# Kernel tuning notes

Hardware: AMD Instinct MI355X
Metric: run time of the kernel (lower is better)

The kernel has to match this reference:

```python
import jax, jax.numpy as jnp
import numpy as np

D_MODEL = 1024
N_HEADS = 16
D_K = D_MODEL // N_HEADS


def setup_inputs() -> dict:
    key = jax.random.key(0)
    ks = jax.random.split(key, 9)
    B, S = 2, 2048
    scale = 1.0 / np.sqrt(D_MODEL)
    inp = {
        "X": jax.random.normal(ks[0], (B, S, D_MODEL), dtype=jnp.float32),
        "Wq": jax.random.normal(ks[1], (D_MODEL, D_MODEL), dtype=jnp.float32) * scale,
        "bq": jnp.zeros((D_MODEL,), dtype=jnp.float32),
        "Wk": jax.random.normal(ks[2], (D_MODEL, D_MODEL), dtype=jnp.float32) * scale,
        "bk": jnp.zeros((D_MODEL,), dtype=jnp.float32),
        "Wv": jax.random.normal(ks[3], (D_MODEL, D_MODEL), dtype=jnp.float32) * scale,
        "bv": jnp.zeros((D_MODEL,), dtype=jnp.float32),
        "Wo": jax.random.normal(ks[4], (D_MODEL, D_MODEL), dtype=jnp.float32) * scale,
        "bo": jnp.zeros((D_MODEL,), dtype=jnp.float32),
    }
    return inp


def reference(X, Wq, bq, Wk, bk, Wv, bv, Wo, bo):
    B, S, _ = X.shape
    # QKV projections (torch Linear: x @ W.T + b; here W stored as [in, out])
    Q = X @ Wq + bq
    K = X @ Wk + bk
    V = X @ Wv + bv
    # [B, S, H, Dk] -> [B, H, S, Dk]
    def split_heads(t):
        return t.reshape(B, S, N_HEADS, D_K).transpose(0, 2, 1, 3)
    Q, K, V = split_heads(Q), split_heads(K), split_heads(V)
    scores = jnp.einsum('bhqd,bhkd->bhqk', Q, K) / jnp.sqrt(jnp.float32(D_K))
    attn = jax.nn.softmax(scores, axis=-1)
    out = jnp.einsum('bhqk,bhkd->bhqd', attn, V)  # [B, H, S, Dk]
    out = out.transpose(0, 2, 1, 3).reshape(B, S, D_MODEL)
    return out @ Wo + bo
```

## Files before the change

### kernel.cpp

```cpp
#include <hip/hip_runtime.h>
#include <hip/hip_bf16.h>


typedef __attribute__((ext_vector_type(8))) short short8;
typedef __attribute__((ext_vector_type(4))) float f32x4;
typedef __attribute__((ext_vector_type(2))) float f32x2;
typedef unsigned short u16;
typedef unsigned int u32;

static __device__ __forceinline__ u16 f2bf(float f) {
    union { float f; u32 u; } c; c.f = f;
    u32 u = c.u;
    u32 r = u + 0x7fffu + ((u >> 16) & 1u);
    return (u16)(r >> 16);
}
static __device__ __forceinline__ float bf2f(u16 x) {
    union { u32 u; float f; } c; c.u = ((u32)x) << 16;
    return c.f;
}

#define GL1(p) ((const __attribute__((address_space(1))) void*)(p))
#define LD3(p) ((__attribute__((address_space(3))) void*)(p))
static __device__ __forceinline__ void gld16(const void* g, void* l) {
    __builtin_amdgcn_global_load_lds(GL1(g), LD3(l), 16, 0, 0);
}

#define Q_PRESCALE 0.18033688011112042f

__global__ __launch_bounds__(256) void prep(
    const float* __restrict__ X, u16* __restrict__ Xb,
    const float* __restrict__ Wq, const float* __restrict__ Wk,
    const float* __restrict__ Wv, const float* __restrict__ Wo,
    const float* __restrict__ bq, const float* __restrict__ bk,
    const float* __restrict__ bv,
    u16* __restrict__ Wqkv, u16* __restrict__ Wto, float* __restrict__ Bp)
{
    int id = blockIdx.x;
    int t = threadIdx.x;
    if (id == 5120) {
        for (int i = t; i < 3072; i += 256) {
            int wsel = i >> 10, c = i & 1023;
            float v = (wsel == 0) ? bq[c] * Q_PRESCALE : (wsel == 1 ? bk[c] : bv[c]);
            Bp[i] = v;
        }
        return;
    }
    if (id >= 1024) {
        int i = (id - 1024) * 1024 + t * 4;
        float4 v = *reinterpret_cast<const float4*>(X + i);
        ushort4 o;
        o.x = f2bf(v.x); o.y = f2bf(v.y); o.z = f2bf(v.z); o.w = f2bf(v.w);
        *reinterpret_cast<ushort4*>(Xb + i) = o;
        return;
    }
    int which = id >> 8;
    const float* W; u16* T; float sc;
    switch (which) {
        case 0: W = Wq; T = Wqkv;                sc = Q_PRESCALE; break;
        case 1: W = Wk; T = Wqkv + 1024 * 1024;  sc = 1.0f; break;
        case 2: W = Wv; T = Wqkv + 2048 * 1024;  sc = 1.0f; break;
        default: W = Wo; T = Wto;                sc = 1.0f; break;
    }
    int rem = id & 255;
    int n0 = (rem & 15) * 64, k0 = (rem >> 4) * 64;
    __shared__ float tile[64][65];
    int r = t / 16, c4 = (t % 16) * 4;
    #pragma unroll
    for (int p = 0; p < 4; p++) {
        int row = p * 16 + r;
        float4 v = *reinterpret_cast<const float4*>(W + (k0 + row) * 1024 + n0 + c4);
        tile[row][c4 + 0] = v.x * sc; tile[row][c4 + 1] = v.y * sc;
        tile[row][c4 + 2] = v.z * sc; tile[row][c4 + 3] = v.w * sc;
    }
    __syncthreads();
    #pragma unroll
    for (int p = 0; p < 4; p++) {
        int nrow = p * 16 + r;
        ushort4 o;
        o.x = f2bf(tile[c4 + 0][nrow]); o.y = f2bf(tile[c4 + 1][nrow]);
        o.z = f2bf(tile[c4 + 2][nrow]); o.w = f2bf(tile[c4 + 3][nrow]);
        *reinterpret_cast<ushort4*>(T + (n0 + nrow) * 1024 + k0 + c4) = o;
    }
}

__global__ __launch_bounds__(256, 3) void gemm_qkv(
    const u16* __restrict__ Xb, const u16* __restrict__ Wqkv,
    const float* __restrict__ Bp,
    u16* __restrict__ Qb, u16* __restrict__ Kb, u16* __restrict__ Vtg)
{
    __shared__ __align__(16) u16 As[2][128 * 32];
    __shared__ __align__(16) u16 Bs[2][128 * 32];
    int t = threadIdx.x;
    int w = t >> 6, lane = t & 63, l15 = lane & 15, quad = lane >> 4;
    int wm = (w >> 1) * 64, wn = (w & 1) * 64;
    int bid = blockIdx.x;
    int row0 = (bid & 31) * 128, col0 = (bid >> 5) * 128;

    int drow = lane >> 2;
    int gc8 = ((lane & 3) ^ (drow & 3) ^ ((drow >> 2) & 3)) * 8;
    int asw = ((quad ^ (l15 & 3) ^ ((l15 >> 2) & 3)) & 3) * 8;

    const u16* Ag = Xb + (row0 + drow) * 1024 + gc8;
    const u16* Bg = Wqkv + (col0 + drow) * 1024 + gc8;

    f32x4 acc[4][4];
    #pragma unroll
    for (int i = 0; i < 4; i++)
        #pragma unroll
        for (int j = 0; j < 4; j++)
            acc[i][j] = (f32x4){0.f, 0.f, 0.f, 0.f};

    #pragma unroll
    for (int q = 0; q < 2; q++) {
        int rr = w * 32 + q * 16;
        gld16(Ag + rr * 1024, &As[0][rr * 32]);
        gld16(Bg + rr * 1024, &Bs[0][rr * 32]);
    }
    for (int kt = 0; kt < 32; kt++) {
        __syncthreads();
        int cur = kt & 1;
        if (kt < 31) {
            int k0 = (kt + 1) * 32;
            #pragma unroll
            for (int q = 0; q < 2; q++) {
                int rr = w * 32 + q * 16;
                gld16(Ag + rr * 1024 + k0, &As[cur ^ 1][rr * 32]);
                gld16(Bg + rr * 1024 + k0, &Bs[cur ^ 1][rr * 32]);
            }
        }
        short8 a[4], b[4];
        #pragma unroll
        for (int i = 0; i < 4; i++)
            a[i] = *reinterpret_cast<const short8*>(&As[cur][(wm + i * 16 + l15) * 32 + asw]);
        #pragma unroll
        for (int j = 0; j < 4; j++)
            b[j] = *reinterpret_cast<const short8*>(&Bs[cur][(wn + j * 16 + l15) * 32 + asw]);
        #pragma unroll
        for (int i = 0; i < 4; i++)
            #pragma unroll
            for (int j = 0; j < 4; j++)
                acc[i][j] = __builtin_amdgcn_mfma_f32_16x16x32_bf16(a[i], b[j], acc[i][j], 0, 0, 0);
    }

    int osel = col0 >> 10;
    if (osel == 2) {
        #pragma unroll
        for (int i = 0; i < 4; i++) {
            int gr = row0 + wm + i * 16 + quad * 4;
            int b_ = gr >> 11, s = gr & 2047;
            #pragma unroll
            for (int j = 0; j < 4; j++) {
                int col = col0 + wn + j * 16 + l15;
                int c = col & 1023, h = c >> 6, d = c & 63;
                float bb = Bp[col];
                ushort4 pk;
                pk.x = f2bf(acc[i][j][0] + bb);
                pk.y = f2bf(acc[i][j][1] + bb);
                pk.z = f2bf(acc[i][j][2] + bb);
                pk.w = f2bf(acc[i][j][3] + bb);
                *reinterpret_cast<ushort4*>(&Vtg[((b_ * 16 + h) * 64 + d) * 2048 + s]) = pk;
            }
        }
    } else {
        u16* dst = osel ? Kb : Qb;
        #pragma unroll
        for (int i = 0; i < 4; i++) {
            int rowb = row0 + wm + i * 16 + quad * 4;
            #pragma unroll
            for (int j = 0; j < 4; j++) {
                int col = col0 + wn + j * 16 + l15;
                int c = col & 1023, h = c >> 6, d = c & 63;
                float bb = Bp[col];
                #pragma unroll
                for (int r = 0; r < 4; r++) {
                    int gr = rowb + r;
                    int b_ = gr >> 11, s = gr & 2047;
                    dst[(((b_ << 4) + h) * 2048 + s) * 64 + d] = f2bf(acc[i][j][r] + bb);
                }
            }
        }
    }
}

__global__ __launch_bounds__(256) void attn(
    const u16* __restrict__ Qb, const u16* __restrict__ Kb,
    const u16* __restrict__ Vtg, u16* __restrict__ Opart, float* __restrict__ Lsum)
{
    int bid = blockIdx.x;
    int bh = bid & 31, sp = (bid >> 5) & 3, qt = bid >> 7;
    int b_ = bh >> 4, h = bh & 15;
    const u16* Qp = Qb + bh * (2048 * 64);
    const u16* Kp = Kb + bh * (2048 * 64);
    const u16* Vp = Vtg + bh * (64 * 2048);
    u16* Op = Opart + sp * (4096 * 1024);
    float* Lp = Lsum + sp * (32 * 2048) + bh * 2048;

    __shared__ __align__(16) u16 Ks[64 * 64];
    __shared__ __align__(16) u16 Vt[64 * 64];
    __shared__ __align__(16) u16 Ps[128 * 64];

    int t = threadIdx.x, w = t >> 6, lane = t & 63, l15 = lane & 15, quad = lane >> 4;

    short8 qf[2][2];
    #pragma unroll
    for (int f = 0; f < 2; f++)
        #pragma unroll
        for (int ds = 0; ds < 2; ds++)
            qf[f][ds] = *reinterpret_cast<const short8*>(
                &Qp[(qt * 128 + w * 32 + f * 16 + l15) * 64 + ds * 32 + quad * 8]);

    int di = lane >> 3;
    int dc8 = ((lane & 7) ^ di) * 8;

    int rl = l15 & 7, rh = l15 >> 3;
    int koff[4][2];
    #pragma unroll
    for (int j = 0; j < 4; j++)
        #pragma unroll
        for (int ds = 0; ds < 2; ds++)
            koff[j][ds] = (j * 2 + rh) * 512 + rl * 64 + (((ds * 4 + quad) ^ rl) & 7) * 8;

    int pwt[2][4];
    #pragma unroll
    for (int f = 0; f < 2; f++)
        #pragma unroll
        for (int j = 0; j < 4; j++)
            pwt[f][j] = (w * 32 + f * 16 + l15) * 64 +
                        (((2 * j + (quad >> 1)) ^ rl) * 8) + (quad & 1) * 4;
    int prt[2][2];
    #pragma unroll
    for (int f = 0; f < 2; f++)
        #pragma unroll
        for (int ks = 0; ks < 2; ks++)
            prt[f][ks] = (w * 32 + f * 16 + l15) * 64 + (((4 * ks + quad) ^ rl) * 8);

    f32x4 acc[2][4];
    f32x2 lsum2[2] = {(f32x2){0.f, 0.f}, (f32x2){0.f, 0.f}};
    #pragma unroll
    for (int f = 0; f < 2; f++)
        #pragma unroll
        for (int j = 0; j < 4; j++) acc[f][j] = (f32x4){0.f, 0.f, 0.f, 0.f};

    int kb0 = sp * 512;

#define ISSUE_K(KB)                                                          \
    {                                                                        \
        _Pragma("unroll")                                                    \
        for (int sg = 0; sg < 2; sg++) {                                     \
            int seg = w * 2 + sg;                                            \
            gld16(&Kp[((KB) + seg * 8 + di) * 64 + dc8], &Ks[seg * 512]);    \
        }                                                                    \
    }
#define ISSUE_V(KB)                                                          \
    {                                                                        \
        _Pragma("unroll")                                                    \
        for (int sg = 0; sg < 2; sg++) {                                     \
            int seg = w * 2 + sg;                                            \
            gld16(&Vp[(seg * 8 + di) * 2048 + (KB) + dc8], &Vt[seg * 512]);  \
        }                                                                    \
    }

    ISSUE_K(kb0);
    ISSUE_V(kb0);
    __syncthreads();

    for (int kt = 0; kt < 8; kt++) {
        f32x4 sc[2][4];
        __builtin_amdgcn_s_setprio(1);
        #pragma unroll
        for (int j = 0; j < 4; j++) {
            f32x4 s0 = (f32x4){0.f, 0.f, 0.f, 0.f};
            f32x4 s1 = (f32x4){0.f, 0.f, 0.f, 0.f};
            #pragma unroll
            for (int ds = 0; ds < 2; ds++) {
                short8 kf = *reinterpret_cast<const short8*>(&Ks[koff[j][ds]]);
                s0 = __builtin_amdgcn_mfma_f32_16x16x32_bf16(kf, qf[0][ds], s0, 0, 0, 0);
                s1 = __builtin_amdgcn_mfma_f32_16x16x32_bf16(kf, qf[1][ds], s1, 0, 0, 0);
            }
            sc[0][j] = s0; sc[1][j] = s1;
        }
        __builtin_amdgcn_s_setprio(0);

        __syncthreads();
        if (kt < 7)
            ISSUE_K(kb0 + (kt + 1) * 64);

        #pragma unroll
        for (int f = 0; f < 2; f++)
            #pragma unroll
            for (int j = 0; j < 4; j++) {
                float p0 = __builtin_amdgcn_exp2f(sc[f][j][0]);
                float p1 = __builtin_amdgcn_exp2f(sc[f][j][1]);
                float p2 = __builtin_amdgcn_exp2f(sc[f][j][2]);
                float p3 = __builtin_amdgcn_exp2f(sc[f][j][3]);
                lsum2[f] += (f32x2){p0, p1};
                lsum2[f] += (f32x2){p2, p3};
                union { float fv; u32 uv; } c0, c1, c2, c3;
                c0.fv = p0; c1.fv = p1; c2.fv = p2; c3.fv = p3;
                uint2 pk;
                pk.x = (c0.uv >> 16) | (c1.uv & 0xffff0000u);
                pk.y = (c2.uv >> 16) | (c3.uv & 0xffff0000u);
                *reinterpret_cast<uint2*>(&Ps[pwt[f][j]]) = pk;
            }

        __builtin_amdgcn_s_setprio(1);
        #pragma unroll
        for (int ks = 0; ks < 2; ks++) {
            short8 pf0 = *reinterpret_cast<const short8*>(&Ps[prt[0][ks]]);
            short8 pf1 = *reinterpret_cast<const short8*>(&Ps[prt[1][ks]]);
            #pragma unroll
            for (int j = 0; j < 4; j++) {
                short8 vf = *reinterpret_cast<const short8*>(&Vt[koff[j][ks]]);
                acc[0][j] = __builtin_amdgcn_mfma_f32_16x16x32_bf16(pf0, vf, acc[0][j], 0, 0, 0);
                acc[1][j] = __builtin_amdgcn_mfma_f32_16x16x32_bf16(pf1, vf, acc[1][j], 0, 0, 0);
            }
        }
        __builtin_amdgcn_s_setprio(0);

        __syncthreads();
        if (kt < 7)
            ISSUE_V(kb0 + (kt + 1) * 64);
    }
#undef ISSUE_K
#undef ISSUE_V

    #pragma unroll
    for (int f = 0; f < 2; f++) {
        float s = lsum2[f].x + lsum2[f].y;
        s += __shfl_xor(s, 16);
        s += __shfl_xor(s, 32);
        if (quad == 0)
            Lp[qt * 128 + w * 32 + f * 16 + l15] = s;
    }

    #pragma unroll
    for (int f = 0; f < 2; f++)
        #pragma unroll
        for (int j = 0; j < 4; j++)
            #pragma unroll
            for (int r = 0; r < 4; r++) {
                int srow = qt * 128 + w * 32 + f * 16 + quad * 4 + r;
                Op[(b_ * 2048 + srow) * 1024 + h * 64 + j * 16 + l15] = f2bf(acc[f][j][r]);
            }
}

__global__ __launch_bounds__(256) void combine(
    const u16* __restrict__ Op, const float* __restrict__ Ls,
    u16* __restrict__ Ob)
{
    int idx8 = (blockIdx.x * 256 + threadIdx.x) * 8;
    int row = idx8 >> 10, col = idx8 & 1023;
    int b_ = row >> 11, s = row & 2047, h = col >> 6;
    int li = (b_ * 16 + h) * 2048 + s;
    float l = Ls[li] + Ls[li + 65536] + Ls[li + 131072] + Ls[li + 196608];
    float inv = 1.0f / l;
    float accv[8];
    #pragma unroll
    for (int i = 0; i < 8; i++) accv[i] = 0.f;
    #pragma unroll
    for (int p = 0; p < 4; p++) {
        union { uint4 v; u16 s[8]; } ua;
        ua.v = *reinterpret_cast<const uint4*>(&Op[p * 4194304 + idx8]);
        #pragma unroll
        for (int i = 0; i < 8; i++) accv[i] += bf2f(ua.s[i]);
    }
    union { uint4 v; u16 s[8]; } uo;
    #pragma unroll
    for (int i = 0; i < 8; i++) uo.s[i] = f2bf(accv[i] * inv);
    *reinterpret_cast<uint4*>(&Ob[idx8]) = uo.v;
}

__global__ __launch_bounds__(256, 3) void gemm_out(
    const u16* __restrict__ Ob, const u16* __restrict__ Wto,
    const float* __restrict__ bo, float* __restrict__ out)
{
    __shared__ __align__(16) u16 As[2][128 * 32];
    __shared__ __align__(16) u16 Bs[2][128 * 32];
    int t = threadIdx.x;
    int w = t >> 6, lane = t & 63, l15 = lane & 15, quad = lane >> 4;
    int wm = (w >> 1) * 64, wn = (w & 1) * 64;
    int bid = blockIdx.x;
    int row0 = (bid & 31) * 128, col0 = (bid >> 5) * 128;

    int drow = lane >> 2;
    int gc8 = ((lane & 3) ^ (drow & 3) ^ ((drow >> 2) & 3)) * 8;
    int asw = ((quad ^ (l15 & 3) ^ ((l15 >> 2) & 3)) & 3) * 8;

    const u16* Ag = Ob + (row0 + drow) * 1024 + gc8;
    const u16* Bg = Wto + (col0 + drow) * 1024 + gc8;

    f32x4 acc[4][4];
    #pragma unroll
    for (int i = 0; i < 4; i++)
        #pragma unroll
        for (int j = 0; j < 4; j++)
            acc[i][j] = (f32x4){0.f, 0.f, 0.f, 0.f};

    #pragma unroll
    for (int q = 0; q < 2; q++) {
        int rr = w * 32 + q * 16;
        gld16(Ag + rr * 1024, &As[0][rr * 32]);
        gld16(Bg + rr * 1024, &Bs[0][rr * 32]);
    }
    for (int kt = 0; kt < 32; kt++) {
        __syncthreads();
        int cur = kt & 1;
        if (kt < 31) {
            int k0 = (kt + 1) * 32;
            #pragma unroll
            for (int q = 0; q < 2; q++) {
                int rr = w * 32 + q * 16;
                gld16(Ag + rr * 1024 + k0, &As[cur ^ 1][rr * 32]);
                gld16(Bg + rr * 1024 + k0, &Bs[cur ^ 1][rr * 32]);
            }
        }
        short8 a[4], b[4];
        #pragma unroll
        for (int i = 0; i < 4; i++)
            a[i] = *reinterpret_cast<const short8*>(&As[cur][(wm + i * 16 + l15) * 32 + asw]);
        #pragma unroll
        for (int j = 0; j < 4; j++)
            b[j] = *reinterpret_cast<const short8*>(&Bs[cur][(wn + j * 16 + l15) * 32 + asw]);
        #pragma unroll
        for (int i = 0; i < 4; i++)
            #pragma unroll
            for (int j = 0; j < 4; j++)
                acc[i][j] = __builtin_amdgcn_mfma_f32_16x16x32_bf16(a[i], b[j], acc[i][j], 0, 0, 0);
    }
    #pragma unroll
    for (int i = 0; i < 4; i++) {
        int rowb = row0 + wm + i * 16 + quad * 4;
        #pragma unroll
        for (int j = 0; j < 4; j++) {
            int col = col0 + wn + j * 16 + l15;
            float bb = bo[col];
            #pragma unroll
            for (int r = 0; r < 4; r++)
                out[(rowb + r) * 1024 + col] = acc[i][j][r] + bb;
        }
    }
}

extern "C" void kernel_launch(void* const* d_in, const int* in_sizes, int n_in,
                              void* d_out, int out_size, void* d_ws, size_t ws_size,
                              hipStream_t stream) {
    const float* X  = (const float*)d_in[0];
    const float* Wq = (const float*)d_in[1];
    const float* bq = (const float*)d_in[2];
    const float* Wk = (const float*)d_in[3];
    const float* bk = (const float*)d_in[4];
    const float* Wv = (const float*)d_in[5];
    const float* bv = (const float*)d_in[6];
    const float* Wo = (const float*)d_in[7];
    const float* bo = (const float*)d_in[8];
    float* out = (float*)d_out;

    char* ws = (char*)d_ws;
    u16* Xb    = (u16*)(ws);
    u16* Ob    = (u16*)(ws);
    u16* Wqkv  = (u16*)(ws + (8u  << 20));
    u16* Wto   = (u16*)(ws + (14u << 20));
    float* Bp  = (float*)(ws + (16u << 20));
    u16* Qb    = (u16*)(ws + (17u << 20));
    u16* Kb    = (u16*)(ws + (25u << 20));
    u16* Vtg   = (u16*)(ws + (33u << 20));
    u16* Op    = (u16*)(ws + (41u << 20));
    float* Ls  = (float*)(ws + (73u << 20));

    prep     <<<5121, 256, 0, stream>>>(X, Xb, Wq, Wk, Wv, Wo, bq, bk, bv, Wqkv, Wto, Bp);
    gemm_qkv <<<768, 256, 0, stream>>>(Xb, Wqkv, Bp, Qb, Kb, Vtg);
    attn     <<<2048, 256, 0, stream>>>(Qb, Kb, Vtg, Op, Ls);
    combine  <<<2048, 256, 0, stream>>>(Op, Ls, Ob);
    gemm_out <<<256, 256, 0, stream>>>(Ob, Wto, bo, out);
}
```

Measured before the change: 202.3 us.

## Drop split-K attention partials and fold softmax normalization into attention epilogue

The attention kernel no longer splits each head's key range into four independent partitions. Each block now loops over all 2048 keys and normalizes its output by the row sum before writing bf16 directly to Ob. This removes the separate combine kernel and the round-trip of four bf16 partial outputs plus row sums through global memory. The cost is a 4x smaller grid with 4x longer per-block loops, which reduces parallelism and latency hiding across CUs.

```diff
diff --git a/kernel.cpp b/kernel.cpp
--- a/kernel.cpp
+++ b/kernel.cpp
@@ -184,16 +184,14 @@
 
 __global__ __launch_bounds__(256) void attn(
     const u16* __restrict__ Qb, const u16* __restrict__ Kb,
-    const u16* __restrict__ Vtg, u16* __restrict__ Opart, float* __restrict__ Lsum)
+    const u16* __restrict__ Vtg, u16* __restrict__ Ob)
 {
     int bid = blockIdx.x;
-    int bh = bid & 31, sp = (bid >> 5) & 3, qt = bid >> 7;
+    int bh = bid & 31, qt = bid >> 5;
     int b_ = bh >> 4, h = bh & 15;
     const u16* Qp = Qb + bh * (2048 * 64);
     const u16* Kp = Kb + bh * (2048 * 64);
     const u16* Vp = Vtg + bh * (64 * 2048);
-    u16* Op = Opart + sp * (4096 * 1024);
-    float* Lp = Lsum + sp * (32 * 2048) + bh * 2048;
 
     __shared__ __align__(16) u16 Ks[64 * 64];
     __shared__ __align__(16) u16 Vt[64 * 64];
@@ -240,8 +238,6 @@
     for (int f = 0; f < 2; f++)
         #pragma unroll
         for (int j = 0; j < 4; j++) acc[f][j] = (f32x4){0.f, 0.f, 0.f, 0.f};
-
-    int kb0 = sp * 512;
 
 #define ISSUE_K(KB)                                                          \
     {                                                                        \
@@ -260,11 +256,12 @@
         }                                                                    \
     }
 
-    ISSUE_K(kb0);
-    ISSUE_V(kb0);
+    ISSUE_K(0);
+    ISSUE_V(0);
     __syncthreads();
 
-    for (int kt = 0; kt < 8; kt++) {
+    for (int kt = 0; kt < 32; kt++) {
+        int kbase = kt * 64;
         f32x4 sc[2][4];
         __builtin_amdgcn_s_setprio(1);
         #pragma unroll
@@ -282,8 +279,8 @@
         __builtin_amdgcn_s_setprio(0);
 
         __syncthreads();
-        if (kt < 7)
-            ISSUE_K(kb0 + (kt + 1) * 64);
+        if (kt < 31)
+            ISSUE_K(kbase + 64);
 
         #pragma unroll
         for (int f = 0; f < 2; f++)
@@ -318,56 +315,32 @@
         __builtin_amdgcn_s_setprio(0);
 
         __syncthreads();
-        if (kt < 7)
-            ISSUE_V(kb0 + (kt + 1) * 64);
+        if (kt < 31)
+            ISSUE_V(kbase + 64);
     }
 #undef ISSUE_K
 #undef ISSUE_V
 
+    float invf[2];
     #pragma unroll
     for (int f = 0; f < 2; f++) {
         float s = lsum2[f].x + lsum2[f].y;
         s += __shfl_xor(s, 16);
         s += __shfl_xor(s, 32);
-        if (quad == 0)
-            Lp[qt * 128 + w * 32 + f * 16 + l15] = s;
+        invf[f] = 1.0f / s;
     }
 
     #pragma unroll
     for (int f = 0; f < 2; f++)
         #pragma unroll
-        for (int j = 0; j < 4; j++)
-            #pragma unroll
-            for (int r = 0; r < 4; r++) {
-                int srow = qt * 128 + w * 32 + f * 16 + quad * 4 + r;
-                Op[(b_ * 2048 + srow) * 1024 + h * 64 + j * 16 + l15] = f2bf(acc[f][j][r]);
-            }
-}
-
-__global__ __launch_bounds__(256) void combine(
-    const u16* __restrict__ Op, const float* __restrict__ Ls,
-    u16* __restrict__ Ob)
-{
-    int idx8 = (blockIdx.x * 256 + threadIdx.x) * 8;
-    int row = idx8 >> 10, col = idx8 & 1023;
-    int b_ = row >> 11, s = row & 2047, h = col >> 6;
-    int li = (b_ * 16 + h) * 2048 + s;
-    float l = Ls[li] + Ls[li + 65536] + Ls[li + 131072] + Ls[li + 196608];
-    float inv = 1.0f / l;
-    float accv[8];
-    #pragma unroll
-    for (int i = 0; i < 8; i++) accv[i] = 0.f;
-    #pragma unroll
-    for (int p = 0; p < 4; p++) {
-        union { uint4 v; u16 s[8]; } ua;
-        ua.v = *reinterpret_cast<const uint4*>(&Op[p * 4194304 + idx8]);
-        #pragma unroll
-        for (int i = 0; i < 8; i++) accv[i] += bf2f(ua.s[i]);
-    }
-    union { uint4 v; u16 s[8]; } uo;
-    #pragma unroll
-    for (int i = 0; i < 8; i++) uo.s[i] = f2bf(accv[i] * inv);
-    *reinterpret_cast<uint4*>(&Ob[idx8]) = uo.v;
+        for (int r = 0; r < 4; r++) {
+            float iv = __shfl(invf[f], quad * 4 + r);
+            int srow = qt * 128 + w * 32 + f * 16 + quad * 4 + r;
+            #pragma unroll
+            for (int j = 0; j < 4; j++)
+                Ob[(b_ * 2048 + srow) * 1024 + h * 64 + j * 16 + l15] =
+                    f2bf(acc[f][j][r] * iv);
+        }
 }
 
 __global__ __launch_bounds__(256, 3) void gemm_out(
@@ -464,12 +437,9 @@
     u16* Qb    = (u16*)(ws + (17u << 20));
     u16* Kb    = (u16*)(ws + (25u << 20));
     u16* Vtg   = (u16*)(ws + (33u << 20));
-    u16* Op    = (u16*)(ws + (41u << 20));
-    float* Ls  = (float*)(ws + (73u << 20));
 
     prep     <<<5121, 256, 0, stream>>>(X, Xb, Wq, Wk, Wv, Wo, bq, bk, bv, Wqkv, Wto, Bp);
     gemm_qkv <<<768, 256, 0, stream>>>(Xb, Wqkv, Bp, Qb, Kb, Vtg);
-    attn     <<<2048, 256, 0, stream>>>(Qb, Kb, Vtg, Op, Ls);
-    combine  <<<2048, 256, 0, stream>>>(Op, Ls, Ob);
+    attn     <<<512, 256, 0, stream>>>(Qb, Kb, Vtg, Ob);
     gemm_out <<<256, 256, 0, stream>>>(Ob, Wto, bo, out);
 }
```

After: 196.7 us. 1.03x faster.
